# Kernel tuning notes

Measured on AMD Instinct MI355X. Metric: run time of the kernel, lower is better.

The kernel has to match this reference:

```python
import jax, jax.numpy as jnp
import numpy as np

B, C, H, W = 4, 256, 64, 64
C8 = C // 8


def setup_inputs() -> dict:
    key = jax.random.key(0)
    ks = jax.random.split(key, 6)
    s_in = 1.0 / np.sqrt(C)
    return {
        "topview": jax.random.normal(ks[0], (B, C, H, W), dtype=jnp.float32),
        "sideview": jax.random.normal(ks[1], (B, C, H, W), dtype=jnp.float32),
        "Wq": jax.random.normal(ks[2], (C8, C), dtype=jnp.float32) * s_in,
        "bq": jnp.zeros((C8,), dtype=jnp.float32),
        "Wk": jax.random.normal(ks[3], (C8, C), dtype=jnp.float32) * s_in,
        "bk": jnp.zeros((C8,), dtype=jnp.float32),
        "Wv": jax.random.normal(ks[4], (C, C), dtype=jnp.float32) * s_in,
        "bv": jnp.zeros((C,), dtype=jnp.float32),
    }


def _conv1x1(x, Wt, b):
    # 1x1 conv == per-pixel channel matmul. x: [B,C,H,W], Wt: [O,C] -> [B,O,H,W]
    return jnp.einsum("bchw,oc->bohw", x, Wt) + b[None, :, None, None]


def reference(topview, sideview, Wq, bq, Wk, bk, Wv, bv):
    b, c, h, w = topview.shape
    n = h * w
    q = _conv1x1(topview, Wq, bq).reshape(b, -1, n).transpose(0, 2, 1)   # [B,N,C8]
    k = _conv1x1(sideview, Wk, bk).reshape(b, -1, n)                      # [B,C8,N]
    v = _conv1x1(sideview, Wv, bv).reshape(b, c, n).transpose(0, 2, 1)    # [B,N,C]
    energy = jax.nn.softmax(jnp.einsum("bnc,bcm->bnm", q, k), axis=2)     # [B,N,N]
    trans = jnp.einsum("bnm,bmc->bnc", energy, v).transpose(0, 2, 1)      # [B,C,N]
    return topview + trans.reshape(b, c, h, w)
```

## Files before the change

### kernel.cpp

```cpp
#include <hip/hip_runtime.h>
#include <math.h>

#define B_   4
#define C_   256
#define C8_  32
#define N_   4096
#define NT   64
#define SMAX 40.0f

typedef float f32x4 __attribute__((ext_vector_type(4)));
typedef short s16x8 __attribute__((ext_vector_type(8)));
typedef short s16x4 __attribute__((ext_vector_type(4)));

static __device__ __forceinline__ short f2bf(float x) {
    unsigned u = __builtin_bit_cast(unsigned, x);
    u = (u + 0x7fffu + ((u >> 16) & 1u)) >> 16;
    return (short)u;
}
static __device__ __forceinline__ float bf2f(short s) {
    unsigned u = ((unsigned)(unsigned short)s) << 16;
    return __builtin_bit_cast(float, u);
}


__global__ __launch_bounds__(256) void convert_w(
    const float* __restrict__ Wq, const float* __restrict__ Wk,
    const float* __restrict__ Wv, short* __restrict__ Wqc,
    short* __restrict__ Wkc, short* __restrict__ Wvc)
{
    const int t = threadIdx.x, lane = t & 63, tq = lane >> 4, tc = lane & 15;
    int task = blockIdx.x * 4 + (t >> 6);
    const float* src; short* dst; int p;
    if (task < 16)      { src = Wq; dst = Wqc; p = task; }
    else if (task < 32) { src = Wk; dst = Wkc; p = task - 16; }
    else                { src = Wv; dst = Wvc; p = task - 32; }
    const int of = p >> 3, kk = p & 7;
    const float* s = src + (size_t)(of * 16 + tc) * 256 + kk * 32 + tq * 8;
    float4 a = *(const float4*)s, c4 = *(const float4*)(s + 4);
    float vv[8] = {a.x, a.y, a.z, a.w, c4.x, c4.y, c4.z, c4.w};
    s16x8 hv, lv;
#pragma unroll
    for (int j = 0; j < 8; ++j) {
        short h = f2bf(vv[j]);
        hv[j] = h;
        lv[j] = f2bf(vv[j] - bf2f(h));
    }
    short* d = dst + (size_t)p * 1024 + lane * 8;
    *(s16x8*)d = hv;
    *(s16x8*)(d + 512) = lv;
}

template <int MODE>
__global__ __launch_bounds__(256) void proj_gemm(
    const float* __restrict__ X, const short* __restrict__ Wc,
    const float* __restrict__ bias, short* __restrict__ Y)
{
    __shared__ __align__(16) char sm[36864];
    const int t = threadIdx.x;
    const int lane = t & 63, tq = lane >> 4, tc = lane & 15, w = t >> 6;
    const int nb = blockIdx.x, b = blockIdx.y;
    const float* Xb = X + (size_t)b * C_ * N_ + nb * 64;

    const int cpl = t >> 6;
    const int nl  = t & 63;
    const int wmask = ((nl >> 3) & 3) << 4;

    constexpr int NO = MODE ? 8 : 2;
    constexpr int NN = MODE ? 2 : 1;
    f32x4 acc[NO][NN];
#pragma unroll
    for (int i = 0; i < NO; ++i)
#pragma unroll
        for (int j = 0; j < NN; ++j) acc[i][j] = {0.f, 0.f, 0.f, 0.f};

    float2 xr[4];
#pragma unroll
    for (int p = 0; p < 4; ++p) {
        int cp = p * 4 + cpl;
        const float* s = Xb + (size_t)(cp * 2) * N_ + nl;
        xr[p] = {s[0], s[N_]};
    }

    int buf = 0;
    for (int kk = 0; kk < 8; ++kk) {
#pragma unroll
        for (int p = 0; p < 4; ++p) {
            int cp = p * 4 + cpl;
            short h0 = f2bf(xr[p].x), h1 = f2bf(xr[p].y);
            short l0 = f2bf(xr[p].x - bf2f(h0)), l1 = f2bf(xr[p].y - bf2f(h1));
            unsigned hp = (unsigned short)h0 | ((unsigned)(unsigned short)h1 << 16);
            unsigned lp = (unsigned short)l0 | ((unsigned)(unsigned short)l1 << 16);
            int off = (cp * 4) ^ wmask;
            *(unsigned*)(sm + buf * 10240 + nl * 80 + off)        = hp;
            *(unsigned*)(sm + buf * 10240 + 5120 + nl * 80 + off) = lp;
        }
        __syncthreads();
        if (kk < 7) {
#pragma unroll
            for (int p = 0; p < 4; ++p) {
                int cp = p * 4 + cpl;
                const float* s = Xb + (size_t)((kk + 1) * 32 + cp * 2) * N_ + nl;
                xr[p] = {s[0], s[N_]};
            }
        }

        if constexpr (MODE == 0) {
            const int row = w * 16 + tc;
            const int roff = (tq * 16) ^ (((row >> 3) & 3) << 4);
            s16x8 bh = *(const s16x8*)(sm + buf * 10240 + row * 80 + roff);
            s16x8 bl = *(const s16x8*)(sm + buf * 10240 + 5120 + row * 80 + roff);
#pragma unroll
            for (int of = 0; of < 2; ++of) {
                const short* wp = Wc + (size_t)((of * 8 + kk) * 2) * 512 + lane * 8;
                s16x8 ah = *(const s16x8*)wp;
                s16x8 al = *(const s16x8*)(wp + 512);
                acc[of][0] = __builtin_amdgcn_mfma_f32_16x16x32_bf16(ah, bh, acc[of][0], 0, 0, 0);
                acc[of][0] = __builtin_amdgcn_mfma_f32_16x16x32_bf16(ah, bl, acc[of][0], 0, 0, 0);
                acc[of][0] = __builtin_amdgcn_mfma_f32_16x16x32_bf16(al, bh, acc[of][0], 0, 0, 0);
            }
        } else {
            const int nh = w >> 1, oh = w & 1;
            s16x8 ah[2], al[2];
#pragma unroll
            for (int nfl = 0; nfl < 2; ++nfl) {
                int row = nh * 32 + nfl * 16 + tc;
                int roff = (tq * 16) ^ (((row >> 3) & 3) << 4);
                ah[nfl] = *(const s16x8*)(sm + buf * 10240 + row * 80 + roff);
                al[nfl] = *(const s16x8*)(sm + buf * 10240 + 5120 + row * 80 + roff);
            }
#pragma unroll
            for (int ofl = 0; ofl < 8; ++ofl) {
                int of = oh * 8 + ofl;
                const short* wp = Wc + (size_t)((of * 8 + kk) * 2) * 512 + lane * 8;
                s16x8 bh = *(const s16x8*)wp;
                s16x8 bl = *(const s16x8*)(wp + 512);
#pragma unroll
                for (int nfl = 0; nfl < 2; ++nfl) {
                    acc[ofl][nfl] = __builtin_amdgcn_mfma_f32_16x16x32_bf16(ah[nfl], bh, acc[ofl][nfl], 0, 0, 0);
                    acc[ofl][nfl] = __builtin_amdgcn_mfma_f32_16x16x32_bf16(ah[nfl], bl, acc[ofl][nfl], 0, 0, 0);
                    acc[ofl][nfl] = __builtin_amdgcn_mfma_f32_16x16x32_bf16(al[nfl], bh, acc[ofl][nfl], 0, 0, 0);
                }
            }
        }
        buf ^= 1;
    }

    const int swz = (tc & 7) << 4;
    if constexpr (MODE == 0) {
        char* S = sm + 20480 + w * 2048;
#pragma unroll
        for (int of = 0; of < 2; ++of)
            *(f32x4*)(S + tc * 128 + ((of * 64 + tq * 16) ^ swz)) = acc[of][0];
        float4 bA = *(const float4*)(bias + tq * 8);
        float4 bB = *(const float4*)(bias + tq * 8 + 4);
        f32x4 r0 = *(const f32x4*)(S + tc * 128 + ((tq * 32) ^ swz));
        f32x4 r1 = *(const f32x4*)(S + tc * 128 + ((tq * 32 + 16) ^ swz));
        float v[8] = {r0[0] + bA.x, r0[1] + bA.y, r0[2] + bA.z, r0[3] + bA.w,
                      r1[0] + bB.x, r1[1] + bB.y, r1[2] + bB.z, r1[3] + bB.w};
        s16x8 hv, lv;
#pragma unroll
        for (int j = 0; j < 8; ++j) {
            short h = f2bf(v[j]);
            hv[j] = h;
            lv[j] = f2bf(v[j] - bf2f(h));
        }
        const int nf = nb * 4 + w;
        short* dst = Y + (size_t)b * 256 * 2 * 512 + (size_t)(nf * 2) * 512 + lane * 8;
        *(s16x8*)dst = hv;
        *(s16x8*)(dst + 512) = lv;
    } else {
        const int nh = w >> 1, oh = w & 1;
#pragma unroll
        for (int ofl = 0; ofl < 8; ++ofl) {
            int of = oh * 8 + ofl;
            char* S = sm + 20480 + w * 4096 + (ofl & 1) * 2048;
            float bv = bias[of * 16 + tc];
#pragma unroll
            for (int nfl = 0; nfl < 2; ++nfl) {
                f32x4 v = acc[ofl][nfl];
                v[0] += bv; v[1] += bv; v[2] += bv; v[3] += bv;
                *(f32x4*)(S + tc * 128 + ((nfl * 64 + tq * 16) ^ swz)) = v;
            }
            f32x4 r0 = *(const f32x4*)(S + tc * 128 + ((tq * 32) ^ swz));
            f32x4 r1 = *(const f32x4*)(S + tc * 128 + ((tq * 32 + 16) ^ swz));
            s16x8 st;
#pragma unroll
            for (int j = 0; j < 4; ++j) { st[j] = f2bf(r0[j]); st[j + 4] = f2bf(r1[j]); }
            short* dst = Y + (size_t)b * (64 * 2 * 16 * 512)
                       + (size_t)((nb * 2 + nh) * 16 + of) * 512 + lane * 8;
            *(s16x8*)dst = st;
        }
    }
}

#define PS_BUF 4096
#define LS_OFF 8192
#define SMEM_BYTES (8192 + 512)

__global__ __launch_bounds__(512, 4) void attn_kernel(
    const short* __restrict__ Qc, const short* __restrict__ Kc,
    const short* __restrict__ Vc, const float* __restrict__ TOP,
    float* __restrict__ OUT)
{
    __shared__ __align__(16) char smem[SMEM_BYTES];

    const int flat = blockIdx.x;
    const int work = (flat & 7) * 64 + (flat >> 3);
    const int b  = work >> 7;
    const int n0 = (work & 127) * 32;

    const int t    = threadIdx.x;
    const int lane = t & 63;
    const int w    = t >> 6;
    const int tq   = lane >> 4;
    const int tc   = lane & 15;
    const int wm   = w >> 1, wn2 = w & 1;

    const short* Qb = Qc + (size_t)b * 256 * 2 * 512;
    const short* Kb = Kc + (size_t)b * 256 * 2 * 512;
    const short* Vb = Vc + (size_t)b * 64 * 2 * 16 * 512;

    const int nf = (n0 >> 4) + wn2;
    const s16x8 qhi = *(const s16x8*)(Qb + ((size_t)nf * 2 + 0) * 512 + lane * 8);
    const s16x8 qlo = *(const s16x8*)(Qb + ((size_t)nf * 2 + 1) * 512 + lane * 8);

    const int nS   = wn2 * 16 + tc;
    const int pswr = (nS * 128 + wm * 32 + tq * 8) ^ ((nS & 7) << 4);
    const int prd00 = ((tc * 128) + 0  + tq * 16) ^ ((tc & 7) << 4);
    const int prd01 = ((tc * 128) + 64 + tq * 16) ^ ((tc & 7) << 4);

    float l_run = 0.f;
    f32x4 acc00 = {0,0,0,0}, acc01 = {0,0,0,0}, acc10 = {0,0,0,0}, acc11 = {0,0,0,0};

    s16x8 kch = *(const s16x8*)(Kb + ((size_t)(0 * 4 + wm) * 2 + 0) * 512 + lane * 8);
    s16x8 kcl = *(const s16x8*)(Kb + ((size_t)(0 * 4 + wm) * 2 + 1) * 512 + lane * 8);
    s16x8 vc00 = *(const s16x8*)(Vb + ((size_t)(0 * 2 + 0) * 16 + w * 2 + 0) * 512 + lane * 8);
    s16x8 vc01 = *(const s16x8*)(Vb + ((size_t)(0 * 2 + 0) * 16 + w * 2 + 1) * 512 + lane * 8);
    s16x8 vc10 = *(const s16x8*)(Vb + ((size_t)(0 * 2 + 1) * 16 + w * 2 + 0) * 512 + lane * 8);
    s16x8 vc11 = *(const s16x8*)(Vb + ((size_t)(0 * 2 + 1) * 16 + w * 2 + 1) * 512 + lane * 8);

    int buf = 0;
    for (int kt = 0; kt < NT; ++kt) {
        const int kn = (kt + 1) & (NT - 1);
        s16x8 knh = *(const s16x8*)(Kb + ((size_t)(kn * 4 + wm) * 2 + 0) * 512 + lane * 8);
        s16x8 knl = *(const s16x8*)(Kb + ((size_t)(kn * 4 + wm) * 2 + 1) * 512 + lane * 8);
        s16x8 vn00 = *(const s16x8*)(Vb + ((size_t)(kn * 2 + 0) * 16 + w * 2 + 0) * 512 + lane * 8);
        s16x8 vn01 = *(const s16x8*)(Vb + ((size_t)(kn * 2 + 0) * 16 + w * 2 + 1) * 512 + lane * 8);
        s16x8 vn10 = *(const s16x8*)(Vb + ((size_t)(kn * 2 + 1) * 16 + w * 2 + 0) * 512 + lane * 8);
        s16x8 vn11 = *(const s16x8*)(Vb + ((size_t)(kn * 2 + 1) * 16 + w * 2 + 1) * 512 + lane * 8);

        f32x4 T = {0.f, 0.f, 0.f, 0.f};
        T = __builtin_amdgcn_mfma_f32_16x16x32_bf16(kch, qhi, T, 0, 0, 0);
        T = __builtin_amdgcn_mfma_f32_16x16x32_bf16(kch, qlo, T, 0, 0, 0);
        T = __builtin_amdgcn_mfma_f32_16x16x32_bf16(kcl, qhi, T, 0, 0, 0);

        s16x4 pb;
        float ps = 0.f;
#pragma unroll
        for (int r = 0; r < 4; ++r) {
            short h = f2bf(__expf(T[r] - SMAX));
            pb[r] = h;
            ps += bf2f(h);
        }
        l_run += ps;
        *(s16x4*)(smem + buf * PS_BUF + pswr) = pb;

        asm volatile("s_waitcnt lgkmcnt(0)" ::: "memory");
        __builtin_amdgcn_s_barrier();

        const char* pbase = smem + buf * PS_BUF;
        s16x8 a00 = *(const s16x8*)(pbase + prd00);
        s16x8 a01 = *(const s16x8*)(pbase + prd01);
        s16x8 a10 = *(const s16x8*)(pbase + prd00 + 2048);
        s16x8 a11 = *(const s16x8*)(pbase + prd01 + 2048);
        acc00 = __builtin_amdgcn_mfma_f32_16x16x32_bf16(a00, vc00, acc00, 0, 0, 0);
        acc00 = __builtin_amdgcn_mfma_f32_16x16x32_bf16(a01, vc10, acc00, 0, 0, 0);
        acc01 = __builtin_amdgcn_mfma_f32_16x16x32_bf16(a00, vc01, acc01, 0, 0, 0);
        acc01 = __builtin_amdgcn_mfma_f32_16x16x32_bf16(a01, vc11, acc01, 0, 0, 0);
        acc10 = __builtin_amdgcn_mfma_f32_16x16x32_bf16(a10, vc00, acc10, 0, 0, 0);
        acc10 = __builtin_amdgcn_mfma_f32_16x16x32_bf16(a11, vc10, acc10, 0, 0, 0);
        acc11 = __builtin_amdgcn_mfma_f32_16x16x32_bf16(a10, vc01, acc11, 0, 0, 0);
        acc11 = __builtin_amdgcn_mfma_f32_16x16x32_bf16(a11, vc11, acc11, 0, 0, 0);

        kch = knh; kcl = knl;
        vc00 = vn00; vc01 = vn01; vc10 = vn10; vc11 = vn11;
        buf ^= 1;
    }

    float lw = l_run;
    lw += __shfl_xor(lw, 16);
    lw += __shfl_xor(lw, 32);
    float* lsum = (float*)(smem + LS_OFF);
    if (tq == 0) lsum[wm * 32 + nS] = lw;
    __syncthreads();

#pragma unroll
    for (int nfr = 0; nfr < 2; ++nfr) {
        f32x4 lv = {0.f, 0.f, 0.f, 0.f};
#pragma unroll
        for (int g = 0; g < 4; ++g)
            lv += *(const f32x4*)&lsum[g * 32 + nfr * 16 + tq * 4];
        f32x4 linv = {1.f / lv[0], 1.f / lv[1], 1.f / lv[2], 1.f / lv[3]};
#pragma unroll
        for (int half = 0; half < 2; ++half) {
            int c = w * 32 + half * 16 + tc;
            size_t g = ((size_t)b * C_ + c) * N_ + n0 + nfr * 16 + tq * 4;
            float4 tp = *(const float4*)&TOP[g];
            f32x4 o4 = (nfr == 0 ? (half == 0 ? acc00 : acc01)
                                 : (half == 0 ? acc10 : acc11)) * linv;
            float4 st = { tp.x + o4[0], tp.y + o4[1], tp.z + o4[2], tp.w + o4[3] };
            *(float4*)&OUT[g] = st;
        }
    }
}

extern "C" void kernel_launch(void* const* d_in, const int* in_sizes, int n_in,
                              void* d_out, int out_size, void* d_ws, size_t ws_size,
                              hipStream_t stream)
{
    const float* top  = (const float*)d_in[0];
    const float* side = (const float*)d_in[1];
    const float* Wq   = (const float*)d_in[2];
    const float* bq   = (const float*)d_in[3];
    const float* Wk   = (const float*)d_in[4];
    const float* bk   = (const float*)d_in[5];
    const float* Wv   = (const float*)d_in[6];
    const float* bv   = (const float*)d_in[7];
    float* out = (float*)d_out;

    short* Qw  = (short*)d_ws;
    short* Kw  = Qw  + (size_t)B_ * 256 * 2 * 512;
    short* Vw  = Kw  + (size_t)B_ * 256 * 2 * 512;
    short* Wqc = Vw  + (size_t)B_ * 64 * 2 * 16 * 512;
    short* Wkc = Wqc + 2 * 8 * 2 * 512;
    short* Wvc = Wkc + 2 * 8 * 2 * 512;

    convert_w<<<dim3(40), dim3(256), 0, stream>>>(Wq, Wk, Wv, Wqc, Wkc, Wvc);
    proj_gemm<0><<<dim3(64, B_), dim3(256), 0, stream>>>(top,  Wqc, bq, Qw);
    proj_gemm<0><<<dim3(64, B_), dim3(256), 0, stream>>>(side, Wkc, bk, Kw);
    proj_gemm<1><<<dim3(64, B_), dim3(256), 0, stream>>>(side, Wvc, bv, Vw);
    attn_kernel<<<dim3(512), dim3(512), 0, stream>>>(Qw, Kw, Vw, top, out);
}
```

Baseline: 181.1 us.

## Merge Q/K/V projection GEMMs into one launch with full-K shared tile

Replaces three separate projection kernel launches with a single launch whose z-dimension selects the Q, K or V projection. Each block now loads the whole 256-channel input tile into 80KB of shared memory once, split into bf16 hi/lo parts, instead of double-buffering K chunks. The V path is retiled so each wave covers 4 output fragments by 4 pixel fragments. This cuts launch overhead and lets all three projections run concurrently, at the cost of large shared memory per block (lower occupancy) and no load/compute overlap.

Result: faster. 176.5 us (-2.6%).

```diff
diff --git a/kernel.cpp b/kernel.cpp
--- a/kernel.cpp
+++ b/kernel.cpp
@@ -20,6 +20,9 @@
 static __device__ __forceinline__ float bf2f(short s) {
     unsigned u = ((unsigned)(unsigned short)s) << 16;
     return __builtin_bit_cast(float, u);
+}
+static __device__ __forceinline__ unsigned pk2(short a, short b) {
+    return (unsigned)(unsigned short)a | ((unsigned)(unsigned short)b << 16);
 }
 
 
@@ -50,111 +53,74 @@
     *(s16x8*)(d + 512) = lv;
 }
 
-template <int MODE>
-__global__ __launch_bounds__(256) void proj_gemm(
-    const float* __restrict__ X, const short* __restrict__ Wc,
-    const float* __restrict__ bias, short* __restrict__ Y)
+__global__ __launch_bounds__(256) void proj_all(
+    const float* __restrict__ top, const float* __restrict__ side,
+    const short* __restrict__ Wqc, const short* __restrict__ Wkc,
+    const short* __restrict__ Wvc,
+    const float* __restrict__ bq, const float* __restrict__ bk,
+    const float* __restrict__ bv,
+    short* __restrict__ Qw, short* __restrict__ Kw, short* __restrict__ Vw)
 {
-    __shared__ __align__(16) char sm[36864];
+    __shared__ __align__(16) char sm[81920];
     const int t = threadIdx.x;
     const int lane = t & 63, tq = lane >> 4, tc = lane & 15, w = t >> 6;
-    const int nb = blockIdx.x, b = blockIdx.y;
+    const int nb = blockIdx.x, b = blockIdx.y, sel = blockIdx.z;
+
+    const float* X = (sel == 0) ? top : side;
     const float* Xb = X + (size_t)b * C_ * N_ + nb * 64;
 
-    const int cpl = t >> 6;
-    const int nl  = t & 63;
-    const int wmask = ((nl >> 3) & 3) << 4;
-
-    constexpr int NO = MODE ? 8 : 2;
-    constexpr int NN = MODE ? 2 : 1;
-    f32x4 acc[NO][NN];
-#pragma unroll
-    for (int i = 0; i < NO; ++i)
-#pragma unroll
-        for (int j = 0; j < NN; ++j) acc[i][j] = {0.f, 0.f, 0.f, 0.f};
-
-    float2 xr[4];
-#pragma unroll
-    for (int p = 0; p < 4; ++p) {
-        int cp = p * 4 + cpl;
-        const float* s = Xb + (size_t)(cp * 2) * N_ + nl;
-        xr[p] = {s[0], s[N_]};
-    }
-
-    int buf = 0;
-    for (int kk = 0; kk < 8; ++kk) {
-#pragma unroll
-        for (int p = 0; p < 4; ++p) {
-            int cp = p * 4 + cpl;
-            short h0 = f2bf(xr[p].x), h1 = f2bf(xr[p].y);
-            short l0 = f2bf(xr[p].x - bf2f(h0)), l1 = f2bf(xr[p].y - bf2f(h1));
-            unsigned hp = (unsigned short)h0 | ((unsigned)(unsigned short)h1 << 16);
-            unsigned lp = (unsigned short)l0 | ((unsigned)(unsigned short)l1 << 16);
-            int off = (cp * 4) ^ wmask;
-            *(unsigned*)(sm + buf * 10240 + nl * 80 + off)        = hp;
-            *(unsigned*)(sm + buf * 10240 + 5120 + nl * 80 + off) = lp;
-        }
-        __syncthreads();
-        if (kk < 7) {
-#pragma unroll
-            for (int p = 0; p < 4; ++p) {
-                int cp = p * 4 + cpl;
-                const float* s = Xb + (size_t)((kk + 1) * 32 + cp * 2) * N_ + nl;
-                xr[p] = {s[0], s[N_]};
-            }
-        }
-
-        if constexpr (MODE == 0) {
-            const int row = w * 16 + tc;
-            const int roff = (tq * 16) ^ (((row >> 3) & 3) << 4);
-            s16x8 bh = *(const s16x8*)(sm + buf * 10240 + row * 80 + roff);
-            s16x8 bl = *(const s16x8*)(sm + buf * 10240 + 5120 + row * 80 + roff);
-#pragma unroll
-            for (int of = 0; of < 2; ++of) {
-                const short* wp = Wc + (size_t)((of * 8 + kk) * 2) * 512 + lane * 8;
-                s16x8 ah = *(const s16x8*)wp;
-                s16x8 al = *(const s16x8*)(wp + 512);
-                acc[of][0] = __builtin_amdgcn_mfma_f32_16x16x32_bf16(ah, bh, acc[of][0], 0, 0, 0);
-                acc[of][0] = __builtin_amdgcn_mfma_f32_16x16x32_bf16(ah, bl, acc[of][0], 0, 0, 0);
-                acc[of][0] = __builtin_amdgcn_mfma_f32_16x16x32_bf16(al, bh, acc[of][0], 0, 0, 0);
-            }
-        } else {
-            const int nh = w >> 1, oh = w & 1;
-            s16x8 ah[2], al[2];
-#pragma unroll
-            for (int nfl = 0; nfl < 2; ++nfl) {
-                int row = nh * 32 + nfl * 16 + tc;
-                int roff = (tq * 16) ^ (((row >> 3) & 3) << 4);
-                ah[nfl] = *(const s16x8*)(sm + buf * 10240 + row * 80 + roff);
-                al[nfl] = *(const s16x8*)(sm + buf * 10240 + 5120 + row * 80 + roff);
-            }
-#pragma unroll
-            for (int ofl = 0; ofl < 8; ++ofl) {
-                int of = oh * 8 + ofl;
-                const short* wp = Wc + (size_t)((of * 8 + kk) * 2) * 512 + lane * 8;
-                s16x8 bh = *(const s16x8*)wp;
-                s16x8 bl = *(const s16x8*)(wp + 512);
-#pragma unroll
-                for (int nfl = 0; nfl < 2; ++nfl) {
-                    acc[ofl][nfl] = __builtin_amdgcn_mfma_f32_16x16x32_bf16(ah[nfl], bh, acc[ofl][nfl], 0, 0, 0);
-                    acc[ofl][nfl] = __builtin_amdgcn_mfma_f32_16x16x32_bf16(ah[nfl], bl, acc[ofl][nfl], 0, 0, 0);
-                    acc[ofl][nfl] = __builtin_amdgcn_mfma_f32_16x16x32_bf16(al[nfl], bh, acc[ofl][nfl], 0, 0, 0);
-                }
-            }
-        }
-        buf ^= 1;
-    }
-
-    const int swz = (tc & 7) << 4;
-    if constexpr (MODE == 0) {
-        char* S = sm + 20480 + w * 2048;
-#pragma unroll
-        for (int of = 0; of < 2; ++of)
-            *(f32x4*)(S + tc * 128 + ((of * 64 + tq * 16) ^ swz)) = acc[of][0];
+    {
+        const int nl = t & 63;
+        const int swn = (nl & 7) << 4;
+        const int qb = t >> 6;
+#pragma unroll 4
+        for (int i = 0; i < 16; ++i) {
+            int qd = i * 4 + qb;
+            const float* s = Xb + (size_t)(qd * 4) * N_ + nl;
+            float x0 = s[0], x1 = s[N_], x2 = s[2 * (size_t)N_], x3 = s[3 * (size_t)N_];
+            short h0 = f2bf(x0), h1 = f2bf(x1), h2 = f2bf(x2), h3 = f2bf(x3);
+            short l0 = f2bf(x0 - bf2f(h0)), l1 = f2bf(x1 - bf2f(h1));
+            short l2 = f2bf(x2 - bf2f(h2)), l3 = f2bf(x3 - bf2f(h3));
+            uint2 hp = { pk2(h0, h1), pk2(h2, h3) };
+            uint2 lp = { pk2(l0, l1), pk2(l2, l3) };
+            int off = (nl * 512 + qd * 8) ^ swn;
+            *(uint2*)(sm + off)         = hp;
+            *(uint2*)(sm + 32768 + off) = lp;
+        }
+    }
+    __syncthreads();
+
+    if (sel < 2) {
+        const short* Wc   = sel ? Wkc : Wqc;
+        const float* bias = sel ? bk  : bq;
+        short*       Y    = sel ? Kw  : Qw;
+        f32x4 a0 = {0.f,0.f,0.f,0.f}, a1 = {0.f,0.f,0.f,0.f};
+        const int row = w * 16 + tc;
+        const int rb = row * 512, rx = (row & 7) << 4;
+#pragma unroll
+        for (int kk = 0; kk < 8; ++kk) {
+            int cb = kk * 64 + tq * 16;
+            s16x8 bh = *(const s16x8*)(sm + ((rb + cb) ^ rx));
+            s16x8 bl = *(const s16x8*)(sm + 32768 + ((rb + cb) ^ rx));
+            const short* wp0 = Wc + (size_t)(kk * 2) * 512 + lane * 8;
+            const short* wp1 = Wc + (size_t)((8 + kk) * 2) * 512 + lane * 8;
+            s16x8 ah0 = *(const s16x8*)wp0, al0 = *(const s16x8*)(wp0 + 512);
+            s16x8 ah1 = *(const s16x8*)wp1, al1 = *(const s16x8*)(wp1 + 512);
+            a0 = __builtin_amdgcn_mfma_f32_16x16x32_bf16(ah0, bh, a0, 0, 0, 0);
+            a0 = __builtin_amdgcn_mfma_f32_16x16x32_bf16(ah0, bl, a0, 0, 0, 0);
+            a0 = __builtin_amdgcn_mfma_f32_16x16x32_bf16(al0, bh, a0, 0, 0, 0);
+            a1 = __builtin_amdgcn_mfma_f32_16x16x32_bf16(ah1, bh, a1, 0, 0, 0);
+            a1 = __builtin_amdgcn_mfma_f32_16x16x32_bf16(ah1, bl, a1, 0, 0, 0);
+            a1 = __builtin_amdgcn_mfma_f32_16x16x32_bf16(al1, bh, a1, 0, 0, 0);
+        }
+        char* scr = sm + 65536 + w * 2048;
+        const int sw2 = (tc & 7) << 4;
+        *(f32x4*)(scr + tc * 128 + ((tq * 16) ^ sw2))      = a0;
+        *(f32x4*)(scr + tc * 128 + ((64 + tq * 16) ^ sw2)) = a1;
         float4 bA = *(const float4*)(bias + tq * 8);
         float4 bB = *(const float4*)(bias + tq * 8 + 4);
-        f32x4 r0 = *(const f32x4*)(S + tc * 128 + ((tq * 32) ^ swz));
-        f32x4 r1 = *(const f32x4*)(S + tc * 128 + ((tq * 32 + 16) ^ swz));
+        f32x4 r0 = *(const f32x4*)(scr + tc * 128 + ((tq * 32) ^ sw2));
+        f32x4 r1 = *(const f32x4*)(scr + tc * 128 + ((tq * 32 + 16) ^ sw2));
         float v[8] = {r0[0] + bA.x, r0[1] + bA.y, r0[2] + bA.z, r0[3] + bA.w,
                       r1[0] + bB.x, r1[1] + bB.y, r1[2] + bB.z, r1[3] + bB.w};
         s16x8 hv, lv;
@@ -169,26 +135,58 @@
         *(s16x8*)dst = hv;
         *(s16x8*)(dst + 512) = lv;
     } else {
-        const int nh = w >> 1, oh = w & 1;
-#pragma unroll
-        for (int ofl = 0; ofl < 8; ++ofl) {
-            int of = oh * 8 + ofl;
-            char* S = sm + 20480 + w * 4096 + (ofl & 1) * 2048;
-            float bv = bias[of * 16 + tc];
-#pragma unroll
-            for (int nfl = 0; nfl < 2; ++nfl) {
-                f32x4 v = acc[ofl][nfl];
-                v[0] += bv; v[1] += bv; v[2] += bv; v[3] += bv;
-                *(f32x4*)(S + tc * 128 + ((nfl * 64 + tq * 16) ^ swz)) = v;
+        f32x4 acc[4][4];
+#pragma unroll
+        for (int ol = 0; ol < 4; ++ol)
+#pragma unroll
+            for (int nf = 0; nf < 4; ++nf) acc[ol][nf] = {0.f, 0.f, 0.f, 0.f};
+#pragma unroll
+        for (int kk = 0; kk < 8; ++kk) {
+            int cb = kk * 64 + tq * 16;
+            s16x8 ah[4], al[4];
+#pragma unroll
+            for (int nf = 0; nf < 4; ++nf) {
+                int row = nf * 16 + tc;
+                int o = (row * 512 + cb) ^ ((row & 7) << 4);
+                ah[nf] = *(const s16x8*)(sm + o);
+                al[nf] = *(const s16x8*)(sm + 32768 + o);
             }
-            f32x4 r0 = *(const f32x4*)(S + tc * 128 + ((tq * 32) ^ swz));
-            f32x4 r1 = *(const f32x4*)(S + tc * 128 + ((tq * 32 + 16) ^ swz));
-            s16x8 st;
-#pragma unroll
-            for (int j = 0; j < 4; ++j) { st[j] = f2bf(r0[j]); st[j + 4] = f2bf(r1[j]); }
-            short* dst = Y + (size_t)b * (64 * 2 * 16 * 512)
-                       + (size_t)((nb * 2 + nh) * 16 + of) * 512 + lane * 8;
-            *(s16x8*)dst = st;
+#pragma unroll
+            for (int ol = 0; ol < 4; ++ol) {
+                int of = w * 4 + ol;
+                const short* wp = Wvc + (size_t)((of * 8 + kk) * 2) * 512 + lane * 8;
+                s16x8 bh = *(const s16x8*)wp, bl = *(const s16x8*)(wp + 512);
+#pragma unroll
+                for (int nf = 0; nf < 4; ++nf) {
+                    acc[ol][nf] = __builtin_amdgcn_mfma_f32_16x16x32_bf16(ah[nf], bh, acc[ol][nf], 0, 0, 0);
+                    acc[ol][nf] = __builtin_amdgcn_mfma_f32_16x16x32_bf16(ah[nf], bl, acc[ol][nf], 0, 0, 0);
+                    acc[ol][nf] = __builtin_amdgcn_mfma_f32_16x16x32_bf16(al[nf], bh, acc[ol][nf], 0, 0, 0);
+                }
+            }
+        }
+        char* scr = sm + 65536 + w * 4096;
+        const int sw2 = (tc & 7) << 4;
+        short* Vbp = Vw + (size_t)b * (64 * 2 * 16 * 512);
+#pragma unroll
+        for (int ol = 0; ol < 4; ++ol) {
+            int of = w * 4 + ol;
+            float bvv = bv[of * 16 + tc];
+#pragma unroll
+            for (int nf = 0; nf < 4; ++nf) {
+                f32x4 v = acc[ol][nf];
+                v[0] += bvv; v[1] += bvv; v[2] += bvv; v[3] += bvv;
+                *(f32x4*)(scr + tc * 256 + ((nf * 64 + tq * 16) ^ sw2)) = v;
+            }
+#pragma unroll
+            for (int k2 = 0; k2 < 2; ++k2) {
+                f32x4 r0 = *(const f32x4*)(scr + tc * 256 + ((k2 * 128 + tq * 32) ^ sw2));
+                f32x4 r1 = *(const f32x4*)(scr + tc * 256 + ((k2 * 128 + tq * 32 + 16) ^ sw2));
+                s16x8 st;
+#pragma unroll
+                for (int j = 0; j < 4; ++j) { st[j] = f2bf(r0[j]); st[j + 4] = f2bf(r1[j]); }
+                short* dst = Vbp + (size_t)((nb * 2 + k2) * 16 + of) * 512 + lane * 8;
+                *(s16x8*)dst = st;
+            }
         }
     }
 }
@@ -336,8 +334,7 @@
     short* Wvc = Wkc + 2 * 8 * 2 * 512;
 
     convert_w<<<dim3(40), dim3(256), 0, stream>>>(Wq, Wk, Wv, Wqc, Wkc, Wvc);
-    proj_gemm<0><<<dim3(64, B_), dim3(256), 0, stream>>>(top,  Wqc, bq, Qw);
-    proj_gemm<0><<<dim3(64, B_), dim3(256), 0, stream>>>(side, Wkc, bk, Kw);
-    proj_gemm<1><<<dim3(64, B_), dim3(256), 0, stream>>>(side, Wvc, bv, Vw);
+    proj_all<<<dim3(64, B_, 3), dim3(256), 0, stream>>>(
+        top, side, Wqc, Wkc, Wvc, bq, bk, bv, Qw, Kw, Vw);
     attn_kernel<<<dim3(512), dim3(512), 0, stream>>>(Qw, Kw, Vw, top, out);
 }
```
